# Kernel optimization log

Hardware: AMD Instinct MI355X
Metric: run time of the kernel (lower is better)

The kernel has to match this reference:

```python
import jax, jax.numpy as jnp
import numpy as np

C = 1.0          # curvature parameter (constraint <x,x>_L = -1/C)
EPS = 1e-7
N_NODES = 50000
D = 128
N_EDGES = 800000


def _l_inner(u, v):
    # Lorentz (Minkowski) inner product: -u0*v0 + <u_s, v_s>
    return -u[..., 0] * v[..., 0] + jnp.sum(u[..., 1:] * v[..., 1:], axis=-1)


def _proj(x, c=C):
    # recompute time coordinate so x lies on the hyperboloid
    sp = x[:, 1:]
    x0 = jnp.sqrt(1.0 / c + jnp.sum(sp * sp, axis=-1, keepdims=True))
    return jnp.concatenate([x0, sp], axis=-1)


def _logmap0(x, c=C):
    sqc = jnp.sqrt(c)
    x0, sp = x[:, :1], x[:, 1:]
    y = jnp.clip(sqc * x0, 1.0 + EPS, None)
    d = jnp.arccosh(y) / sqc                                   # geodesic distance to origin
    sn = jnp.clip(jnp.linalg.norm(sp, axis=-1, keepdims=True), EPS, None)
    return jnp.concatenate([jnp.zeros_like(x0), d * sp / sn], axis=-1)


def _expmap0(u, c=C):
    sqc = jnp.sqrt(c)
    sp = u[:, 1:]
    un = jnp.clip(jnp.linalg.norm(sp, axis=-1, keepdims=True), EPS, None)
    th = sqc * un
    x0 = jnp.cosh(th) / sqc
    return jnp.concatenate([x0, jnp.sinh(th) * sp / th], axis=-1)


def setup_inputs() -> dict:
    key = jax.random.key(0)
    k1, k2, k3 = jax.random.split(key, 3)
    x_raw = jax.random.normal(k1, (N_NODES, D), dtype=jnp.float32) * 0.5
    x = _proj(x_raw)  # valid points on the Lorentz manifold
    # xavier-uniform-like scale for (127,127) weight
    lim = float(np.sqrt(6.0 / (2 * (D - 1))))
    weight = jax.random.uniform(k2, (D - 1, D - 1), dtype=jnp.float32, minval=-lim, maxval=lim)
    bias = jnp.zeros((D - 1,), dtype=jnp.float32)
    edge_index = jax.random.randint(k3, (2, N_EDGES), 0, N_NODES, dtype=jnp.int64)
    return {"x": x, "weight": weight, "bias": bias, "edge_index": edge_index}


def reference(x, weight, bias, edge_index):
    c = C
    # ---- HyperbolicLinear (lorentz): log0 -> spatial matmul + bias -> exp0 -> proj
    v = _logmap0(x, c)                         # [N, D], time comp = 0
    out_space = v[:, 1:] @ weight.T + bias     # [N, D-1]
    out = jnp.concatenate([v[:, :1], out_space], axis=-1)
    h = _proj(_expmap0(out, c), c)             # [N, D] on manifold
    # ---- HyperbolicDistAtt: gather -> lorentz distance -> exp(-d)
    row, col = edge_index[0], edge_index[1]
    xi = h[row]                                # [E, D]
    xj = h[col]                                # [E, D]
    inner = _l_inner(xi, xj)                   # [E]
    dist = jnp.arccosh(jnp.clip(-c * inner, 1.0 + EPS, None)) / jnp.sqrt(c)
    att = jnp.exp(-dist)                       # [E]
    # ---- Lorentz centroid: weighted sum then Minkowski-norm normalization
    num = jax.ops.segment_sum(att[:, None] * xj, row, num_segments=h.shape[0])  # [N, D]
    denom = jnp.sqrt(c) * jnp.sqrt(jnp.clip(-_l_inner(num, num), EPS, None))    # [N]
    return num / denom[:, None]
```

## Files before the change

### kernel.cpp

```cpp
#include <hip/hip_runtime.h>
#include <math.h>

#define EPS 1e-7f
#define CAP 64
#define REC_INTS   34
#define REC_USH    68
#define LIST_OFF    4

typedef __attribute__((ext_vector_type(8))) short short8;
typedef __attribute__((ext_vector_type(4))) float floatx4;

__device__ inline short f2bf(float f) {
    union { float f; unsigned u; } v; v.f = f;
    unsigned r = v.u + 0x7FFF + ((v.u >> 16) & 1);
    return (short)(r >> 16);
}

__device__ inline float fast_sqrt(float x) { return __builtin_amdgcn_sqrtf(x); }
__device__ inline float fast_rcp(float x)  { return __builtin_amdgcn_rcpf(x); }
__device__ inline float fast_rsq(float x)  { return __builtin_amdgcn_rsqf(x); }

__global__ __launch_bounds__(256) void prep_w(
    const float* __restrict__ weight, short* __restrict__ wfg,
    int* __restrict__ rec, int N)
{
    int idx = blockIdx.x * 256 + threadIdx.x;
    if (idx < 128 * 128) {
        int j = idx >> 7, k = idx & 127;
        float w = (j < 127 && k >= 1) ? weight[j * 127 + (k - 1)] : 0.0f;
        int tt = j >> 4, cc = j & 15, ss = k >> 5, qq = (k >> 3) & 3, ee = k & 7;
        wfg[(((tt * 4 + ss) * 64) + qq * 16 + cc) * 8 + ee] = f2bf(w);
    }
    if (rec) {
        for (int r = idx; r < N; r += gridDim.x * 256) rec[(size_t)r * REC_INTS] = 0;
    }
}

__global__ __launch_bounds__(256) void transform_mfma(
    const float* __restrict__ x, const short* __restrict__ wfg,
    const float* __restrict__ bias, float* __restrict__ h, int N)
{
    __shared__ __align__(16) short Wf[8 * 4 * 64 * 8];
    __shared__ __align__(16) short Vf[4 * 4 * 64 * 8];

    const int t = threadIdx.x;
    const int lane = t & 63;
    const int wv = t >> 6;
    const int c = lane & 15;
    const int q = lane >> 4;

    {
        const short8* src = (const short8*)wfg;
        short8* dst = (short8*)Wf;
        #pragma unroll
        for (int it = 0; it < 8; ++it) dst[it * 256 + t] = src[it * 256 + t];
    }
    float bvals[8];
    #pragma unroll
    for (int tt = 0; tt < 8; ++tt) {
        int j = tt * 16 + c;
        bvals[tt] = (j < 127) ? bias[j] : 0.0f;
    }
    __syncthreads();

    const short8* wfp = (const short8*)Wf;
    const short8* vfp = (const short8*)Vf + wv * 256;
    short8* vw = (short8*)Vf;

    const int nchunks = (N + 63) >> 6;
    for (int chunk = blockIdx.x; chunk < nchunks; chunk += gridDim.x) {
        const int base = chunk * 64;

        {
            int nl = t >> 2;
            int qt = t & 3;
            int n = base + nl;
            const float4* xr = (const float4*)(x + (size_t)n * 128 + qt * 32);
            float4 xv[8];
            if (n < N) {
                #pragma unroll
                for (int g = 0; g < 8; ++g) xv[g] = xr[g];
            } else {
                #pragma unroll
                for (int g = 0; g < 8; ++g) xv[g] = make_float4(0, 0, 0, 0);
            }
            float ss = 0.0f;
            #pragma unroll
            for (int g = 0; g < 8; ++g)
                ss += xv[g].x * xv[g].x + xv[g].y * xv[g].y +
                      xv[g].z * xv[g].z + xv[g].w * xv[g].w;
            float x0 = xv[0].x;
            if (qt == 0) ss -= x0 * x0;
            ss += __shfl_xor(ss, 1, 64);
            ss += __shfl_xor(ss, 2, 64);
            x0 = __shfl(x0, lane & ~3, 64);
            float sn = fmaxf(fast_sqrt(ss), EPS);
            float xc = fmaxf(x0, 1.0f + EPS);
            float dd = __logf(xc + fast_sqrt(xc * xc - 1.0f));
            float coef = dd * fast_rcp(sn);
            int wreg = nl >> 4, cn = nl & 15;
            #pragma unroll
            for (int g = 0; g < 4; ++g) {
                float4 a = xv[2 * g], b = xv[2 * g + 1];
                short8 pk;
                pk[0] = f2bf(coef * a.x); pk[1] = f2bf(coef * a.y);
                pk[2] = f2bf(coef * a.z); pk[3] = f2bf(coef * a.w);
                pk[4] = f2bf(coef * b.x); pk[5] = f2bf(coef * b.y);
                pk[6] = f2bf(coef * b.z); pk[7] = f2bf(coef * b.w);
                vw[wreg * 256 + qt * 64 + g * 16 + cn] = pk;
            }
        }

        floatx4 acc[8];
        #pragma unroll
        for (int tt = 0; tt < 8; ++tt) acc[tt] = (floatx4){0, 0, 0, 0};
        #pragma unroll
        for (int s = 0; s < 4; ++s) {
            short8 af = vfp[s * 64 + lane];
            #pragma unroll
            for (int tt = 0; tt < 8; ++tt) {
                short8 bf = wfp[(tt * 4 + s) * 64 + lane];
                acc[tt] = __builtin_amdgcn_mfma_f32_16x16x32_bf16(af, bf, acc[tt], 0, 0, 0);
            }
        }

        float rs[4] = {0, 0, 0, 0};
        #pragma unroll
        for (int tt = 0; tt < 8; ++tt) {
            #pragma unroll
            for (int r = 0; r < 4; ++r) {
                float v = acc[tt][r] + bvals[tt];
                acc[tt][r] = v;
                rs[r] += v * v;
            }
        }
        #pragma unroll
        for (int r = 0; r < 4; ++r) {
            rs[r] += __shfl_xor(rs[r], 1, 64);
            rs[r] += __shfl_xor(rs[r], 2, 64);
            rs[r] += __shfl_xor(rs[r], 4, 64);
            rs[r] += __shfl_xor(rs[r], 8, 64);
        }
        int nodebase = base + wv * 16 + q * 4;
        #pragma unroll
        for (int r = 0; r < 4; ++r) {
            int n = nodebase + r;
            if (n < N) {
                float th = fmaxf(fast_sqrt(rs[r]), EPS);
                float ex = __expf(th);
                float sc_big = (ex - fast_rcp(ex)) * 0.5f * fast_rcp(th);
                float sc_small = 1.0f + th * th * (1.0f / 6.0f);
                float scale = (th < 1e-3f) ? sc_small : sc_big;
                float* hr = h + (size_t)n * 128;
                #pragma unroll
                for (int tt = 0; tt < 8; ++tt) {
                    int j = tt * 16 + c;
                    if (j < 127) hr[1 + j] = scale * acc[tt][r];
                    else         hr[0] = fast_sqrt(1.0f + scale * scale * rs[r]);
                }
            }
        }
    }
}

__global__ __launch_bounds__(256) void scatter_cap(
    const int* __restrict__ rows, const int* __restrict__ cols,
    int* __restrict__ rec, int E)
{
    int base = blockIdx.x * 1024 + (int)threadIdx.x;
    int r[4], c[4], p[4];
    bool val[4];
    #pragma unroll
    for (int e = 0; e < 4; ++e) {
        int i = base + 256 * e;
        val[e] = i < E;
        r[e] = 0; c[e] = 0;
        if (val[e]) {
            r[e] = __builtin_nontemporal_load(rows + i);
            c[e] = __builtin_nontemporal_load(cols + i);
        }
    }
    #pragma unroll
    for (int e = 0; e < 4; ++e)
        if (val[e]) p[e] = atomicAdd(rec + (size_t)r[e] * REC_INTS, 1);
    #pragma unroll
    for (int e = 0; e < 4; ++e)
        if (val[e] && p[e] < CAP)
            ((ushort*)rec)[(size_t)r[e] * REC_USH + LIST_OFF + p[e]] = (ushort)c[e];
}

__global__ __launch_bounds__(256) void agg_cap(
    const float* __restrict__ h, const int* __restrict__ rec,
    float* __restrict__ out, int N)
{
    int wid = (int)((blockIdx.x * 256u + threadIdx.x) >> 6);
    int nw = (int)(gridDim.x * 4u);
    int lane = threadIdx.x & 63;
    int q = lane >> 4;
    int i = lane & 15;

    for (int n = wid; n < N; n += nw) {
        const ushort* lst = (const ushort*)rec + (size_t)n * REC_USH + LIST_OFF;
        int ec = (int)lst[lane];
        int deg = rec[(size_t)n * REC_INTS];
        if (deg > CAP) deg = CAP;

        const float4* hn = (const float4*)(h + (size_t)n * 128) + 2 * i;
        float4 xa = hn[0], xb = hn[1];
        float xa0 = (i == 0) ? -xa.x : xa.x;
        float acc[8] = {0, 0, 0, 0, 0, 0, 0, 0};

        for (int kb = 0; kb < deg; kb += 32) {
            int k0 = kb + q;
            bool v[8];
            int cc[8];
            #pragma unroll
            for (int e = 0; e < 8; ++e) {
                int kk = k0 + 4 * e;
                v[e] = kk < deg;
                cc[e] = __shfl(ec, kk, 64);
            }
            float4 A[8], B[8];
            #pragma unroll
            for (int e = 0; e < 8; ++e) {
                A[e] = make_float4(0, 0, 0, 0);
                B[e] = make_float4(0, 0, 0, 0);
                if (v[e]) {
                    const float4* p = (const float4*)(h + (size_t)cc[e] * 128) + 2 * i;
                    A[e] = p[0]; B[e] = p[1];
                }
            }
            float s[8];
            #pragma unroll
            for (int e = 0; e < 8; ++e) {
                s[e] = xa0 * A[e].x + xa.y * A[e].y + xa.z * A[e].z + xa.w * A[e].w
                     + xb.x * B[e].x + xb.y * B[e].y + xb.z * B[e].z + xb.w * B[e].w;
            }
            #pragma unroll
            for (int o = 1; o <= 8; o <<= 1) {
                #pragma unroll
                for (int e = 0; e < 8; ++e) s[e] += __shfl_xor(s[e], o, 64);
            }
            float att[8];
            #pragma unroll
            for (int e = 0; e < 8; ++e) {
                float z = fmaxf(-s[e], 1.0f + EPS);
                att[e] = v[e] ? fast_rcp(z + fast_sqrt(z * z - 1.0f)) : 0.0f;
            }
            #pragma unroll
            for (int e = 0; e < 8; ++e) {
                acc[0] += att[e] * A[e].x;
                acc[1] += att[e] * A[e].y;
                acc[2] += att[e] * A[e].z;
                acc[3] += att[e] * A[e].w;
                acc[4] += att[e] * B[e].x;
                acc[5] += att[e] * B[e].y;
                acc[6] += att[e] * B[e].z;
                acc[7] += att[e] * B[e].w;
            }
        }

        #pragma unroll
        for (int k = 0; k < 8; ++k) {
            acc[k] += __shfl_xor(acc[k], 16, 64);
            acc[k] += __shfl_xor(acc[k], 32, 64);
        }

        float part = 0.0f;
        #pragma unroll
        for (int k = 0; k < 8; ++k) part -= acc[k] * acc[k];
        if (i == 0) part += 2.0f * acc[0] * acc[0];
        #pragma unroll
        for (int o = 1; o <= 8; o <<= 1) part += __shfl_xor(part, o, 64);
        float inv = fast_rsq(fmaxf(part, EPS));

        if (q == 0) {
            float4* op = (float4*)(out + (size_t)n * 128) + 2 * i;
            op[0] = make_float4(acc[0] * inv, acc[1] * inv, acc[2] * inv, acc[3] * inv);
            op[1] = make_float4(acc[4] * inv, acc[5] * inv, acc[6] * inv, acc[7] * inv);
        }
    }
}

__global__ __launch_bounds__(256) void hist_kernel(
    const int* __restrict__ rows, int* __restrict__ deg, int E)
{
    int i = blockIdx.x * 256 + threadIdx.x;
    if (i < E) atomicAdd(&deg[rows[i]], 1);
}

__global__ __launch_bounds__(1024) void scan1(
    const int* __restrict__ deg, int* __restrict__ off,
    int* __restrict__ bsum, int N)
{
    __shared__ int wsum[16];
    __shared__ int wexcl[16];
    int i = blockIdx.x * 1024 + threadIdx.x;
    int lane = threadIdx.x & 63, wid = threadIdx.x >> 6;
    int v = (i < N) ? deg[i] : 0;
    int incl = v;
    #pragma unroll
    for (int o = 1; o < 64; o <<= 1) {
        int u = __shfl_up(incl, o, 64);
        if (lane >= o) incl += u;
    }
    if (lane == 63) wsum[wid] = incl;
    __syncthreads();
    if (wid == 0 && lane < 16) {
        int s = wsum[lane];
        int si = s;
        #pragma unroll
        for (int o = 1; o < 16; o <<= 1) {
            int u = __shfl_up(si, o, 64);
            if (lane >= o) si += u;
        }
        wexcl[lane] = si - s;
        if (lane == 15) bsum[blockIdx.x] = si;
    }
    __syncthreads();
    if (i < N) off[i] = wexcl[wid] + incl - v;
}

__global__ __launch_bounds__(64) void scan2(int* __restrict__ bsum, int nb)
{
    int lane = threadIdx.x & 63;
    int v = (lane < nb) ? bsum[lane] : 0;
    int si = v;
    #pragma unroll
    for (int o = 1; o < 64; o <<= 1) {
        int u = __shfl_up(si, o, 64);
        if (lane >= o) si += u;
    }
    if (lane < nb) bsum[lane] = si - v;
}

__global__ __launch_bounds__(1024) void scan3(
    int* __restrict__ off, int* __restrict__ pos,
    const int* __restrict__ bsum, int N, int E)
{
    int i = blockIdx.x * 1024 + threadIdx.x;
    if (i < N) {
        int v = off[i] + bsum[blockIdx.x];
        off[i] = v;
        pos[i] = v;
    }
    if (i == 0) off[N] = E;
}

__global__ __launch_bounds__(256) void scatter_kernel(
    const int* __restrict__ rows, const int* __restrict__ cols,
    int* __restrict__ pos, int* __restrict__ ecol, int E)
{
    int i = blockIdx.x * 256 + threadIdx.x;
    if (i < E) {
        int p = atomicAdd(&pos[rows[i]], 1);
        ecol[p] = cols[i];
    }
}

__global__ __launch_bounds__(256) void agg_kernel(
    const float* __restrict__ h, const int* __restrict__ off,
    const int* __restrict__ ecol, float* __restrict__ out, int N)
{
    int wid = (int)((blockIdx.x * 256u + threadIdx.x) >> 6);
    int nw = (int)(gridDim.x * 4u);
    int lane = threadIdx.x & 63;
    int q = lane >> 4;
    int i = lane & 15;

    for (int n = wid; n < N; n += nw) {
        const float4* hn = (const float4*)(h + (size_t)n * 128) + 2 * i;
        float4 xa = hn[0], xb = hn[1];
        float xa0 = (i == 0) ? -xa.x : xa.x;
        float acc[8] = {0, 0, 0, 0, 0, 0, 0, 0};
        int e0 = off[n], e1 = off[n + 1];

        int e = e0 + q;
        for (; e + 4 < e1; e += 8) {
            int c0 = ecol[e];
            int c1 = ecol[e + 4];
            const float4* p0 = (const float4*)(h + (size_t)c0 * 128) + 2 * i;
            const float4* p1 = (const float4*)(h + (size_t)c1 * 128) + 2 * i;
            float4 a0 = p0[0], b0 = p0[1];
            float4 a1 = p1[0], b1 = p1[1];
            float s0 = xa0 * a0.x + xa.y * a0.y + xa.z * a0.z + xa.w * a0.w
                     + xb.x * b0.x + xb.y * b0.y + xb.z * b0.z + xb.w * b0.w;
            float s1 = xa0 * a1.x + xa.y * a1.y + xa.z * a1.z + xa.w * a1.w
                     + xb.x * b1.x + xb.y * b1.y + xb.z * b1.z + xb.w * b1.w;
            #pragma unroll
            for (int o = 1; o <= 8; o <<= 1) {
                s0 += __shfl_xor(s0, o, 64);
                s1 += __shfl_xor(s1, o, 64);
            }
            float z0 = fmaxf(-s0, 1.0f + EPS);
            float z1 = fmaxf(-s1, 1.0f + EPS);
            float att0 = fast_rcp(z0 + fast_sqrt(z0 * z0 - 1.0f));
            float att1 = fast_rcp(z1 + fast_sqrt(z1 * z1 - 1.0f));
            acc[0] += att0 * a0.x + att1 * a1.x;
            acc[1] += att0 * a0.y + att1 * a1.y;
            acc[2] += att0 * a0.z + att1 * a1.z;
            acc[3] += att0 * a0.w + att1 * a1.w;
            acc[4] += att0 * b0.x + att1 * b1.x;
            acc[5] += att0 * b0.y + att1 * b1.y;
            acc[6] += att0 * b0.z + att1 * b1.z;
            acc[7] += att0 * b0.w + att1 * b1.w;
        }
        if (e < e1) {
            int c0 = ecol[e];
            const float4* p0 = (const float4*)(h + (size_t)c0 * 128) + 2 * i;
            float4 a0 = p0[0], b0 = p0[1];
            float s0 = xa0 * a0.x + xa.y * a0.y + xa.z * a0.z + xa.w * a0.w
                     + xb.x * b0.x + xb.y * b0.y + xb.z * b0.z + xb.w * b0.w;
            #pragma unroll
            for (int o = 1; o <= 8; o <<= 1) s0 += __shfl_xor(s0, o, 64);
            float z0 = fmaxf(-s0, 1.0f + EPS);
            float att0 = fast_rcp(z0 + fast_sqrt(z0 * z0 - 1.0f));
            acc[0] += att0 * a0.x;
            acc[1] += att0 * a0.y;
            acc[2] += att0 * a0.z;
            acc[3] += att0 * a0.w;
            acc[4] += att0 * b0.x;
            acc[5] += att0 * b0.y;
            acc[6] += att0 * b0.z;
            acc[7] += att0 * b0.w;
        }

        #pragma unroll
        for (int k = 0; k < 8; ++k) {
            acc[k] += __shfl_xor(acc[k], 16, 64);
            acc[k] += __shfl_xor(acc[k], 32, 64);
        }

        float part = 0.0f;
        #pragma unroll
        for (int k = 0; k < 8; ++k) part -= acc[k] * acc[k];
        if (i == 0) part += 2.0f * acc[0] * acc[0];
        #pragma unroll
        for (int o = 1; o <= 8; o <<= 1) part += __shfl_xor(part, o, 64);
        float inv = fast_rsq(fmaxf(part, EPS));

        if (q == 0) {
            float4* op = (float4*)(out + (size_t)n * 128) + 2 * i;
            op[0] = make_float4(acc[0] * inv, acc[1] * inv, acc[2] * inv, acc[3] * inv);
            op[1] = make_float4(acc[4] * inv, acc[5] * inv, acc[6] * inv, acc[7] * inv);
        }
    }
}

__global__ __launch_bounds__(256) void edge_kernel(
    const float* __restrict__ h, const int* __restrict__ rows,
    const int* __restrict__ cols, float* __restrict__ num, int E)
{
    int wid = (int)((blockIdx.x * 256u + threadIdx.x) >> 6);
    if (wid >= E) return;
    int lane = threadIdx.x & 63;
    int r = rows[wid];
    int c = cols[wid];
    const float2* h2 = (const float2*)h;
    float2 xi = h2[(size_t)r * 64 + lane];
    float2 xj = h2[(size_t)c * 64 + lane];
    float p = (lane == 0 ? -xi.x * xj.x : xi.x * xj.x) + xi.y * xj.y;
    #pragma unroll
    for (int off = 32; off >= 1; off >>= 1) p += __shfl_xor(p, off, 64);
    float z = fmaxf(-p, 1.0f + EPS);
    float att = fast_rcp(z + fast_sqrt(z * z - 1.0f));
    float* dst = num + (size_t)r * 128 + 2 * lane;
    atomicAdd(dst, att * xj.x);
    atomicAdd(dst + 1, att * xj.y);
}

__global__ __launch_bounds__(256) void norm_kernel(float* __restrict__ num, int N)
{
    int wid = (int)((blockIdx.x * 256u + threadIdx.x) >> 6);
    int nw = (int)((gridDim.x * 256u) >> 6);
    int lane = threadIdx.x & 63;
    for (int n = wid; n < N; n += nw) {
        float2* p2 = (float2*)(num + (size_t)n * 128);
        float2 v = p2[lane];
        float q = (lane == 0) ? (v.x * v.x - v.y * v.y) : (-v.x * v.x - v.y * v.y);
        #pragma unroll
        for (int o = 32; o >= 1; o >>= 1) q += __shfl_xor(q, o, 64);
        float inv = fast_rsq(fmaxf(q, EPS));
        p2[lane] = make_float2(v.x * inv, v.y * inv);
    }
}

extern "C" void kernel_launch(void* const* d_in, const int* in_sizes, int n_in,
                              void* d_out, int out_size, void* d_ws, size_t ws_size,
                              hipStream_t stream)
{
    const float* x      = (const float*)d_in[0];
    const float* weight = (const float*)d_in[1];
    const float* bias   = (const float*)d_in[2];
    const int*   edge   = (const int*)d_in[3];

    const int N = in_sizes[0] / 128;
    const int E = in_sizes[3] / 2;
    const int* rows = edge;
    const int* cols = edge + E;

    char* base = (char*)d_ws;
    float* h   = (float*)base;                       base += (size_t)N * 128 * 4;
    short* wfg = (short*)base;                       base += (size_t)128 * 128 * 2;
    char* rest = base;
    size_t head = (size_t)(rest - (char*)d_ws);

    int* rec = (int*)rest;
    size_t need_cap = head + (size_t)N * REC_INTS * 4;

    int* deg  = (int*)rest;
    int* off  = deg + N;
    int* pos  = off + (N + 1);
    int* bsum = pos + N;
    int* ecol = bsum + 64;
    size_t need_csr = head + ((size_t)N * 3 + 65 + E) * 4;

    const int nchunks = (N + 63) >> 6;

    if (ws_size >= need_cap && N <= 65535) {
        prep_w<<<256, 256, 0, stream>>>(weight, wfg, rec, N);
        transform_mfma<<<nchunks, 256, 0, stream>>>(x, wfg, bias, h, N);
        scatter_cap<<<(E + 1023) / 1024, 256, 0, stream>>>(rows, cols, rec, E);
        agg_cap<<<(N + 3) / 4, 256, 0, stream>>>(h, rec, (float*)d_out, N);
    } else if (ws_size >= need_csr) {
        prep_w<<<256, 256, 0, stream>>>(weight, wfg, deg, N);
        transform_mfma<<<nchunks, 256, 0, stream>>>(x, wfg, bias, h, N);
        const int nsb = (N + 1023) / 1024;
        hist_kernel<<<(E + 255) / 256, 256, 0, stream>>>(rows, deg, E);
        scan1<<<nsb, 1024, 0, stream>>>(deg, off, bsum, N);
        scan2<<<1, 64, 0, stream>>>(bsum, nsb);
        scan3<<<nsb, 1024, 0, stream>>>(off, pos, bsum, N, E);
        scatter_kernel<<<(E + 255) / 256, 256, 0, stream>>>(rows, cols, pos, ecol, E);
        agg_kernel<<<(N + 3) / 4, 256, 0, stream>>>(h, off, ecol, (float*)d_out, N);
    } else {
        prep_w<<<256, 256, 0, stream>>>(weight, wfg, (int*)nullptr, 0);
        transform_mfma<<<nchunks, 256, 0, stream>>>(x, wfg, bias, h, N);
        hipMemsetAsync(d_out, 0, (size_t)out_size * sizeof(float), stream);
        edge_kernel<<<(E + 3) / 4, 256, 0, stream>>>(h, rows, cols, (float*)d_out, E);
        norm_kernel<<<2048, 256, 0, stream>>>((float*)d_out, N);
    }
}
```

Before: 193.4 us.

## Store transformed node features as fp16 and gather half-width rows in aggregation

The transform kernel now writes h in fp16 with the time coordinate moved to the last slot, and the aggregation kernel gathers 16-byte fp16 rows (8 values per lane), processing 4 edges per iteration instead of 8. The weight tile is read straight from global memory instead of being staged in LDS. Self-loop attention is forced to 1. This halves the bytes of the random gathers over h, at the cost of fp16 rounding error in the Lorentz inner products, which can be badly conditioned near the clamp at 1.

```diff
diff --git a/kernel.cpp b/kernel.cpp
--- a/kernel.cpp
+++ b/kernel.cpp
@@ -14,6 +14,15 @@
     union { float f; unsigned u; } v; v.f = f;
     unsigned r = v.u + 0x7FFF + ((v.u >> 16) & 1);
     return (short)(r >> 16);
+}
+__device__ inline ushort f2h(float f) {
+    union { _Float16 h; ushort u; } v; v.h = (_Float16)f; return v.u;
+}
+__device__ inline float h2f_lo(unsigned u) {
+    union { unsigned x; _Float16 h[2]; } v; v.x = u; return (float)v.h[0];
+}
+__device__ inline float h2f_hi(unsigned u) {
+    union { unsigned x; _Float16 h[2]; } v; v.x = u; return (float)v.h[1];
 }
 
 __device__ inline float fast_sqrt(float x) { return __builtin_amdgcn_sqrtf(x); }
@@ -36,11 +45,10 @@
     }
 }
 
-__global__ __launch_bounds__(256) void transform_mfma(
+__global__ __launch_bounds__(256) void transform16(
     const float* __restrict__ x, const short* __restrict__ wfg,
-    const float* __restrict__ bias, float* __restrict__ h, int N)
-{
-    __shared__ __align__(16) short Wf[8 * 4 * 64 * 8];
+    const float* __restrict__ bias, ushort* __restrict__ h16, int N)
+{
     __shared__ __align__(16) short Vf[4 * 4 * 64 * 8];
 
     const int t = threadIdx.x;
@@ -49,21 +57,14 @@
     const int c = lane & 15;
     const int q = lane >> 4;
 
-    {
-        const short8* src = (const short8*)wfg;
-        short8* dst = (short8*)Wf;
-        #pragma unroll
-        for (int it = 0; it < 8; ++it) dst[it * 256 + t] = src[it * 256 + t];
-    }
     float bvals[8];
     #pragma unroll
     for (int tt = 0; tt < 8; ++tt) {
         int j = tt * 16 + c;
         bvals[tt] = (j < 127) ? bias[j] : 0.0f;
     }
-    __syncthreads();
-
-    const short8* wfp = (const short8*)Wf;
+
+    const short8* wfp = (const short8*)wfg;
     const short8* vfp = (const short8*)Vf + wv * 256;
     short8* vw = (short8*)Vf;
 
@@ -151,12 +152,12 @@
                 float sc_big = (ex - fast_rcp(ex)) * 0.5f * fast_rcp(th);
                 float sc_small = 1.0f + th * th * (1.0f / 6.0f);
                 float scale = (th < 1e-3f) ? sc_small : sc_big;
-                float* hr = h + (size_t)n * 128;
+                ushort* hr = h16 + (size_t)n * 128;
                 #pragma unroll
                 for (int tt = 0; tt < 8; ++tt) {
-                    int j = tt * 16 + c;
-                    if (j < 127) hr[1 + j] = scale * acc[tt][r];
-                    else         hr[0] = fast_sqrt(1.0f + scale * scale * rs[r]);
+                    int p = tt * 16 + c;
+                    if (p < 127) hr[p] = f2h(scale * acc[tt][r]);
+                    else hr[127] = f2h(fast_sqrt(1.0f + scale * scale * rs[r]));
                 }
             }
         }
@@ -189,8 +190,8 @@
             ((ushort*)rec)[(size_t)r[e] * REC_USH + LIST_OFF + p[e]] = (ushort)c[e];
 }
 
-__global__ __launch_bounds__(256) void agg_cap(
-    const float* __restrict__ h, const int* __restrict__ rec,
+__global__ __launch_bounds__(256) void agg_cap16(
+    const ushort* __restrict__ h16, const int* __restrict__ rec,
     float* __restrict__ out, int N)
 {
     int wid = (int)((blockIdx.x * 256u + threadIdx.x) >> 6);
@@ -205,58 +206,62 @@
         int deg = rec[(size_t)n * REC_INTS];
         if (deg > CAP) deg = CAP;
 
-        const float4* hn = (const float4*)(h + (size_t)n * 128) + 2 * i;
-        float4 xa = hn[0], xb = hn[1];
-        float xa0 = (i == 0) ? -xa.x : xa.x;
+        uint4 wn = *(const uint4*)(h16 + (size_t)n * 128 + 8 * i);
+        float own[8];
+        own[0] = h2f_lo(wn.x); own[1] = h2f_hi(wn.x);
+        own[2] = h2f_lo(wn.y); own[3] = h2f_hi(wn.y);
+        own[4] = h2f_lo(wn.z); own[5] = h2f_hi(wn.z);
+        own[6] = h2f_lo(wn.w); own[7] = h2f_hi(wn.w);
+        float own7s = (i == 15) ? -own[7] : own[7];
         float acc[8] = {0, 0, 0, 0, 0, 0, 0, 0};
 
-        for (int kb = 0; kb < deg; kb += 32) {
+        for (int kb = 0; kb < deg; kb += 16) {
             int k0 = kb + q;
-            bool v[8];
-            int cc[8];
-            #pragma unroll
-            for (int e = 0; e < 8; ++e) {
+            bool v[4];
+            int cc[4];
+            uint4 w[4];
+            #pragma unroll
+            for (int e = 0; e < 4; ++e) {
                 int kk = k0 + 4 * e;
                 v[e] = kk < deg;
                 cc[e] = __shfl(ec, kk, 64);
-            }
-            float4 A[8], B[8];
-            #pragma unroll
-            for (int e = 0; e < 8; ++e) {
-                A[e] = make_float4(0, 0, 0, 0);
-                B[e] = make_float4(0, 0, 0, 0);
-                if (v[e]) {
-                    const float4* p = (const float4*)(h + (size_t)cc[e] * 128) + 2 * i;
-                    A[e] = p[0]; B[e] = p[1];
-                }
-            }
-            float s[8];
-            #pragma unroll
-            for (int e = 0; e < 8; ++e) {
-                s[e] = xa0 * A[e].x + xa.y * A[e].y + xa.z * A[e].z + xa.w * A[e].w
-                     + xb.x * B[e].x + xb.y * B[e].y + xb.z * B[e].z + xb.w * B[e].w;
+                w[e] = make_uint4(0, 0, 0, 0);
+                if (v[e])
+                    w[e] = *(const uint4*)(h16 + (size_t)cc[e] * 128 + 8 * i);
+            }
+            float g[4][8];
+            #pragma unroll
+            for (int e = 0; e < 4; ++e) {
+                g[e][0] = h2f_lo(w[e].x); g[e][1] = h2f_hi(w[e].x);
+                g[e][2] = h2f_lo(w[e].y); g[e][3] = h2f_hi(w[e].y);
+                g[e][4] = h2f_lo(w[e].z); g[e][5] = h2f_hi(w[e].z);
+                g[e][6] = h2f_lo(w[e].w); g[e][7] = h2f_hi(w[e].w);
+            }
+            float s[4];
+            #pragma unroll
+            for (int e = 0; e < 4; ++e) {
+                s[e] = own[0] * g[e][0] + own[1] * g[e][1]
+                     + own[2] * g[e][2] + own[3] * g[e][3]
+                     + own[4] * g[e][4] + own[5] * g[e][5]
+                     + own[6] * g[e][6] + own7s   * g[e][7];
             }
             #pragma unroll
             for (int o = 1; o <= 8; o <<= 1) {
                 #pragma unroll
-                for (int e = 0; e < 8; ++e) s[e] += __shfl_xor(s[e], o, 64);
-            }
-            float att[8];
-            #pragma unroll
-            for (int e = 0; e < 8; ++e) {
+                for (int e = 0; e < 4; ++e) s[e] += __shfl_xor(s[e], o, 64);
+            }
+            float att[4];
+            #pragma unroll
+            for (int e = 0; e < 4; ++e) {
                 float z = fmaxf(-s[e], 1.0f + EPS);
-                att[e] = v[e] ? fast_rcp(z + fast_sqrt(z * z - 1.0f)) : 0.0f;
-            }
-            #pragma unroll
-            for (int e = 0; e < 8; ++e) {
-                acc[0] += att[e] * A[e].x;
-                acc[1] += att[e] * A[e].y;
-                acc[2] += att[e] * A[e].z;
-                acc[3] += att[e] * A[e].w;
-                acc[4] += att[e] * B[e].x;
-                acc[5] += att[e] * B[e].y;
-                acc[6] += att[e] * B[e].z;
-                acc[7] += att[e] * B[e].w;
+                float a = fast_rcp(z + fast_sqrt(z * z - 1.0f));
+                if (cc[e] == n) a = 1.0f;
+                att[e] = v[e] ? a : 0.0f;
+            }
+            #pragma unroll
+            for (int e = 0; e < 4; ++e) {
+                #pragma unroll
+                for (int m = 0; m < 8; ++m) acc[m] += att[e] * g[e][m];
             }
         }
 
@@ -269,15 +274,138 @@
         float part = 0.0f;
         #pragma unroll
         for (int k = 0; k < 8; ++k) part -= acc[k] * acc[k];
-        if (i == 0) part += 2.0f * acc[0] * acc[0];
+        if (i == 15) part += 2.0f * acc[7] * acc[7];
         #pragma unroll
         for (int o = 1; o <= 8; o <<= 1) part += __shfl_xor(part, o, 64);
         float inv = fast_rsq(fmaxf(part, EPS));
 
         if (q == 0) {
-            float4* op = (float4*)(out + (size_t)n * 128) + 2 * i;
-            op[0] = make_float4(acc[0] * inv, acc[1] * inv, acc[2] * inv, acc[3] * inv);
-            op[1] = make_float4(acc[4] * inv, acc[5] * inv, acc[6] * inv, acc[7] * inv);
+            float* orow = out + (size_t)n * 128;
+            #pragma unroll
+            for (int m = 0; m < 8; ++m) {
+                int p = 8 * i + m;
+                float vv = acc[m] * inv;
+                if (p == 127) orow[0] = vv;
+                else          orow[1 + p] = vv;
+            }
+        }
+    }
+}
+
+__global__ __launch_bounds__(256) void transform_mfma(
+    const float* __restrict__ x, const short* __restrict__ wfg,
+    const float* __restrict__ bias, float* __restrict__ h, int N)
+{
+    __shared__ __align__(16) short Vf[4 * 4 * 64 * 8];
+
+    const int t = threadIdx.x;
+    const int lane = t & 63;
+    const int wv = t >> 6;
+    const int c = lane & 15;
+    const int q = lane >> 4;
+
+    float bvals[8];
+    #pragma unroll
+    for (int tt = 0; tt < 8; ++tt) {
+        int j = tt * 16 + c;
+        bvals[tt] = (j < 127) ? bias[j] : 0.0f;
+    }
+
+    const short8* wfp = (const short8*)wfg;
+    const short8* vfp = (const short8*)Vf + wv * 256;
+    short8* vw = (short8*)Vf;
+
+    const int nchunks = (N + 63) >> 6;
+    for (int chunk = blockIdx.x; chunk < nchunks; chunk += gridDim.x) {
+        const int base = chunk * 64;
+        {
+            int nl = t >> 2;
+            int qt = t & 3;
+            int n = base + nl;
+            const float4* xr = (const float4*)(x + (size_t)n * 128 + qt * 32);
+            float4 xv[8];
+            if (n < N) {
+                #pragma unroll
+                for (int g = 0; g < 8; ++g) xv[g] = xr[g];
+            } else {
+                #pragma unroll
+                for (int g = 0; g < 8; ++g) xv[g] = make_float4(0, 0, 0, 0);
+            }
+            float ss = 0.0f;
+            #pragma unroll
+            for (int g = 0; g < 8; ++g)
+                ss += xv[g].x * xv[g].x + xv[g].y * xv[g].y +
+                      xv[g].z * xv[g].z + xv[g].w * xv[g].w;
+            float x0 = xv[0].x;
+            if (qt == 0) ss -= x0 * x0;
+            ss += __shfl_xor(ss, 1, 64);
+            ss += __shfl_xor(ss, 2, 64);
+            x0 = __shfl(x0, lane & ~3, 64);
+            float sn = fmaxf(fast_sqrt(ss), EPS);
+            float xc = fmaxf(x0, 1.0f + EPS);
+            float dd = __logf(xc + fast_sqrt(xc * xc - 1.0f));
+            float coef = dd * fast_rcp(sn);
+            int wreg = nl >> 4, cn = nl & 15;
+            #pragma unroll
+            for (int g = 0; g < 4; ++g) {
+                float4 a = xv[2 * g], b = xv[2 * g + 1];
+                short8 pk;
+                pk[0] = f2bf(coef * a.x); pk[1] = f2bf(coef * a.y);
+                pk[2] = f2bf(coef * a.z); pk[3] = f2bf(coef * a.w);
+                pk[4] = f2bf(coef * b.x); pk[5] = f2bf(coef * b.y);
+                pk[6] = f2bf(coef * b.z); pk[7] = f2bf(coef * b.w);
+                vw[wreg * 256 + qt * 64 + g * 16 + cn] = pk;
+            }
+        }
+
+        floatx4 acc[8];
+        #pragma unroll
+        for (int tt = 0; tt < 8; ++tt) acc[tt] = (floatx4){0, 0, 0, 0};
+        #pragma unroll
+        for (int s = 0; s < 4; ++s) {
+            short8 af = vfp[s * 64 + lane];
+            #pragma unroll
+            for (int tt = 0; tt < 8; ++tt) {
+                short8 bf = wfp[(tt * 4 + s) * 64 + lane];
+                acc[tt] = __builtin_amdgcn_mfma_f32_16x16x32_bf16(af, bf, acc[tt], 0, 0, 0);
+            }
+        }
+
+        float rs[4] = {0, 0, 0, 0};
+        #pragma unroll
+        for (int tt = 0; tt < 8; ++tt) {
+            #pragma unroll
+            for (int r = 0; r < 4; ++r) {
+                float v = acc[tt][r] + bvals[tt];
+                acc[tt][r] = v;
+                rs[r] += v * v;
+            }
+        }
+        #pragma unroll
+        for (int r = 0; r < 4; ++r) {
+            rs[r] += __shfl_xor(rs[r], 1, 64);
+            rs[r] += __shfl_xor(rs[r], 2, 64);
+            rs[r] += __shfl_xor(rs[r], 4, 64);
+            rs[r] += __shfl_xor(rs[r], 8, 64);
+        }
+        int nodebase = base + wv * 16 + q * 4;
+        #pragma unroll
+        for (int r = 0; r < 4; ++r) {
+            int n = nodebase + r;
+            if (n < N) {
+                float th = fmaxf(fast_sqrt(rs[r]), EPS);
+                float ex = __expf(th);
+                float sc_big = (ex - fast_rcp(ex)) * 0.5f * fast_rcp(th);
+                float sc_small = 1.0f + th * th * (1.0f / 6.0f);
+                float scale = (th < 1e-3f) ? sc_small : sc_big;
+                float* hr = h + (size_t)n * 128;
+                #pragma unroll
+                for (int tt = 0; tt < 8; ++tt) {
+                    int j = tt * 16 + c;
+                    if (j < 127) hr[1 + j] = scale * acc[tt][r];
+                    else         hr[0] = fast_sqrt(1.0f + scale * scale * rs[r]);
+                }
+            }
         }
     }
 }
@@ -499,14 +627,29 @@
     const int* rows = edge;
     const int* cols = edge + E;
 
+    const int nchunks = (N + 63) >> 6;
+
+    {
+        char* base = (char*)d_ws;
+        ushort* h16 = (ushort*)base;                 base += (size_t)N * 128 * 2;
+        short* wfg  = (short*)base;                  base += (size_t)128 * 128 * 2;
+        int* rec    = (int*)base;
+        size_t need_cap = (size_t)((char*)rec - (char*)d_ws) + (size_t)N * REC_INTS * 4;
+
+        if (ws_size >= need_cap && N <= 65535) {
+            prep_w<<<256, 256, 0, stream>>>(weight, wfg, rec, N);
+            transform16<<<nchunks, 256, 0, stream>>>(x, wfg, bias, h16, N);
+            scatter_cap<<<(E + 1023) / 1024, 256, 0, stream>>>(rows, cols, rec, E);
+            agg_cap16<<<(N + 3) / 4, 256, 0, stream>>>(h16, rec, (float*)d_out, N);
+            return;
+        }
+    }
+
     char* base = (char*)d_ws;
     float* h   = (float*)base;                       base += (size_t)N * 128 * 4;
     short* wfg = (short*)base;                       base += (size_t)128 * 128 * 2;
     char* rest = base;
     size_t head = (size_t)(rest - (char*)d_ws);
-
-    int* rec = (int*)rest;
-    size_t need_cap = head + (size_t)N * REC_INTS * 4;
 
     int* deg  = (int*)rest;
     int* off  = deg + N;
@@ -515,14 +658,7 @@
     int* ecol = bsum + 64;
     size_t need_csr = head + ((size_t)N * 3 + 65 + E) * 4;
 
-    const int nchunks = (N + 63) >> 6;
-
-    if (ws_size >= need_cap && N <= 65535) {
-        prep_w<<<256, 256, 0, stream>>>(weight, wfg, rec, N);
-        transform_mfma<<<nchunks, 256, 0, stream>>>(x, wfg, bias, h, N);
-        scatter_cap<<<(E + 1023) / 1024, 256, 0, stream>>>(rows, cols, rec, E);
-        agg_cap<<<(N + 3) / 4, 256, 0, stream>>>(h, rec, (float*)d_out, N);
-    } else if (ws_size >= need_csr) {
+    if (ws_size >= need_csr) {
         prep_w<<<256, 256, 0, stream>>>(weight, wfg, deg, N);
         transform_mfma<<<nchunks, 256, 0, stream>>>(x, wfg, bias, h, N);
         const int nsb = (N + 1023) / 1024;
```

Measured after the change: 175.1 us. 9.5% less time.
